# Optimization experiments

Hardware: AMD Instinct MI355X
Metric: run time of the kernel (lower is better)

## Reference

```python
import jax, jax.numpy as jnp
import numpy as np
from jax import lax

DN = ('NCHW', 'OIHW', 'NCHW')
BN_EPS = 1e-5


def _conv(x, w, pad):
    # pad: list of (lo, hi) for H, W
    return lax.conv_general_dilated(x, w, (1, 1), pad, dimension_numbers=DN)


def _grid_sample_bilinear(img, grid):
    """F.grid_sample(img, grid, align_corners=True, padding_mode='zeros').
    img: [N,C,H,W], grid: [N,Ho,Wo,2] with (x,y) in [-1,1]."""
    N, C, H, W = img.shape
    gx, gy = grid[..., 0], grid[..., 1]
    # align_corners=True mapping to pixel coords
    ix = (gx + 1.0) * 0.5 * (W - 1)
    iy = (gy + 1.0) * 0.5 * (H - 1)
    x0 = jnp.floor(ix)
    y0 = jnp.floor(iy)
    x1 = x0 + 1.0
    y1 = y0 + 1.0
    # bilinear weights
    wa = (x1 - ix) * (y1 - iy)  # top-left (x0,y0)
    wb = (ix - x0) * (y1 - iy)  # top-right (x1,y0)
    wc = (x1 - ix) * (iy - y0)  # bottom-left (x0,y1)
    wd = (ix - x0) * (iy - y0)  # bottom-right (x1,y1)

    imgc = jnp.transpose(img, (0, 2, 3, 1))  # [N,H,W,C]
    b = jnp.arange(N)[:, None, None]

    def gather(xi, yi):
        valid = (xi >= 0) & (xi <= W - 1) & (yi >= 0) & (yi <= H - 1)
        xc = jnp.clip(xi, 0, W - 1).astype(jnp.int32)
        yc = jnp.clip(yi, 0, H - 1).astype(jnp.int32)
        v = imgc[b, yc, xc]  # [N,Ho,Wo,C]
        return v * valid[..., None].astype(img.dtype)

    out = (gather(x0, y0) * wa[..., None] + gather(x1, y0) * wb[..., None]
           + gather(x0, y1) * wc[..., None] + gather(x1, y1) * wd[..., None])
    return jnp.transpose(out, (0, 3, 1, 2))  # [N,C,Ho,Wo]


def setup_inputs() -> dict:
    key = jax.random.key(0)
    ks = jax.random.split(key, 12)
    N, C1, C2 = 8, 512, 256
    H, W = 64, 64
    x1 = jax.random.normal(ks[0], (N, C1, 2 * H, 2 * W), dtype=jnp.float32)
    x2 = jax.random.normal(ks[1], (N, C2, H, W), dtype=jnp.float32)
    w_change = jax.random.normal(ks[2], (C2, C1, 1, 1), dtype=jnp.float32) * 0.02
    b_change = jax.random.normal(ks[3], (C2,), dtype=jnp.float32) * 0.02
    w_cc1 = jax.random.normal(ks[4], (C2, 2 * C2, 1, 1), dtype=jnp.float32) * 0.02
    bn_gamma = 1.0 + 0.1 * jax.random.normal(ks[5], (C2,), dtype=jnp.float32)
    bn_beta = 0.1 * jax.random.normal(ks[6], (C2,), dtype=jnp.float32)
    bn_mean = 0.1 * jax.random.normal(ks[7], (C2,), dtype=jnp.float32)
    bn_var = jax.random.uniform(ks[8], (C2,), dtype=jnp.float32, minval=0.5, maxval=1.5)
    w_cc2 = jax.random.normal(ks[9], (4, C2, 3, 3), dtype=jnp.float32) * 0.02
    return {"x1": x1, "x2": x2, "w_change": w_change, "b_change": b_change,
            "w_cc1": w_cc1, "bn_gamma": bn_gamma, "bn_beta": bn_beta,
            "bn_mean": bn_mean, "bn_var": bn_var, "w_cc2": w_cc2}


def reference(x1, x2, w_change, b_change, w_cc1, bn_gamma, bn_beta, bn_mean, bn_var, w_cc2):
    # MaxPool2d(2,2)
    x1p = lax.reduce_window(x1, -jnp.inf, lax.max, (1, 1, 2, 2), (1, 1, 2, 2), 'VALID')
    # change: 1x1 conv with bias
    x1c = _conv(x1p, w_change, [(0, 0), (0, 0)]) + b_change[None, :, None, None]
    # concat + concat_conv (1x1 conv -> BN(eval) -> ReLU -> 3x3 conv)
    x = jnp.concatenate([x1c, x2], axis=1)
    x = _conv(x, w_cc1, [(0, 0), (0, 0)])
    inv = lax.rsqrt(bn_var + BN_EPS)
    x = (x - bn_mean[None, :, None, None]) * (inv * bn_gamma)[None, :, None, None] + bn_beta[None, :, None, None]
    x = jax.nn.relu(x)
    flow = _conv(x, w_cc2, [(1, 1), (1, 1)])  # [N,4,H,W]
    flow1 = flow[:, :2]
    flow2 = flow[:, 2:]

    N, _, H, W = x1c.shape
    # base grid: [...,0]=x over width, [...,1]=y over height
    xs = jnp.linspace(-1.0, 1.0, W, dtype=x1c.dtype)
    ys = jnp.linspace(-1.0, 1.0, H, dtype=x1c.dtype)
    base = jnp.stack(jnp.meshgrid(xs, ys, indexing='xy'), axis=-1)  # [H,W,2]
    norm = jnp.array([(W - 1) / 2.0, (H - 1) / 2.0], dtype=x1c.dtype)

    grid1 = base[None] + jnp.transpose(flow1, (0, 2, 3, 1)) / norm
    grid2 = base[None] + jnp.transpose(flow2, (0, 2, 3, 1)) / norm

    u1 = _grid_sample_bilinear(x1c, grid1)
    u2 = _grid_sample_bilinear(x2, grid2)
    return u1 + u2
```

## Files before the change

kernel.cpp:

```cpp
#include <hip/hip_runtime.h>
#include <hip/hip_bf16.h>

#define NB 8
#define C1 512
#define C2 256
#define HWSZ 4096
#define BN_EPS 1e-5f
#define P2 264

typedef __hip_bfloat16 bf16;
typedef __hip_bfloat162 bf162;
typedef __attribute__((ext_vector_type(8))) short short8v;
typedef __attribute__((ext_vector_type(4))) float f32x4;

static __device__ inline float b2f(bf16 h) { return __bfloat162float(h); }

static __device__ inline unsigned short f2bf(float f) {
  union { bf16 h; unsigned short u; } c;
  c.h = __float2bfloat16(f);
  return c.u;
}

static __device__ inline unsigned pack2(float a, float b) {
  union { unsigned u; bf162 h; } pk;
  pk.h = __float22bfloat162_rn(make_float2(a, b));
  return pk.u;
}

static __device__ inline uint2 pack4(float a, float b, float c, float d) {
  union { uint2 u; bf162 h[2]; } pk;
  pk.h[0] = __float22bfloat162_rn(make_float2(a, b));
  pk.h[1] = __float22bfloat162_rn(make_float2(c, d));
  return pk.u;
}

#define SBARQ() asm volatile("s_waitcnt lgkmcnt(0)\n\ts_barrier" ::: "memory")
#define SBAR()  asm volatile("s_barrier" ::: "memory")
#define LGKM0() asm volatile("s_waitcnt lgkmcnt(0)" ::: "memory")

__global__ __launch_bounds__(256) void k0_swizzle(
    const float* __restrict__ wch, const float* __restrict__ wcc1,
    unsigned short* __restrict__ wchB, unsigned short* __restrict__ wcc1B) {
  const int t = blockIdx.x * 256 + threadIdx.x;
  const int which = t >> 17;
  const int r = t & 131071;
  const int i = r & 7;
  const int lane = (r >> 3) & 63;
  const int ntile = (r >> 9) & 15;
  const int kstep = r >> 13;
  const int ci = kstep * 32 + (lane >> 4) * 8 + i;
  const int co = ntile * 16 + (lane & 15);
  const float* s = which ? wcc1 : wch;
  unsigned short* d = which ? wcc1B : wchB;
  d[r] = f2bf(s[co * 512 + ci]);
}

__global__ __launch_bounds__(256) void k12_fused(
    const float* __restrict__ x1, const float* __restrict__ x2,
    const unsigned short* __restrict__ wchB, const unsigned short* __restrict__ wcc1B,
    const float* __restrict__ bch,
    const float* __restrict__ gamma, const float* __restrict__ beta,
    const float* __restrict__ mean, const float* __restrict__ var,
    bf16* __restrict__ x1c, bf16* __restrict__ xbn) {
  __shared__ unsigned short As[32 * 40];
  __shared__ unsigned short As2[32 * P2];
  const int tid = threadIdx.x;
  const int lane = tid & 63;
  const int wv = tid >> 6;
  const int lrow = lane & 15;
  const int lgrp = lane >> 4;

  const int m0g = blockIdx.x * 32;
  const int n = m0g >> 12;
  const int hw0 = m0g & 4095;
  const int h = hw0 >> 6;
  const int w0 = hw0 & 63;

  f32x4 acc[2][4];
#pragma unroll
  for (int mt = 0; mt < 2; ++mt)
#pragma unroll
    for (int nt = 0; nt < 4; ++nt) acc[mt][nt] = (f32x4){0.f, 0.f, 0.f, 0.f};

  const int pmi = tid & 15;
  const int ms = pmi * 2;
  const int ch0 = (tid >> 4) * 2;

  const float* x1p = x1 + (size_t)n * C1 * 16384 + (size_t)(2 * h) * 128 + 2 * (w0 + ms);

  float4 t0, b0, t1, b1;
#define LOADA(K0_) do { \
    const float* p_ = x1p + (size_t)((K0_) + ch0) * 16384; \
    t0 = *(const float4*)p_;            b0 = *(const float4*)(p_ + 128); \
    t1 = *(const float4*)(p_ + 16384);  b1 = *(const float4*)(p_ + 16384 + 128); \
  } while (0)
#define POOLA(U0_, U1_) do { \
    U0_ = pack2(fmaxf(fmaxf(t0.x, t0.y), fmaxf(b0.x, b0.y)), \
                fmaxf(fmaxf(t1.x, t1.y), fmaxf(b1.x, b1.y))); \
    U1_ = pack2(fmaxf(fmaxf(t0.z, t0.w), fmaxf(b0.z, b0.w)), \
                fmaxf(fmaxf(t1.z, t1.w), fmaxf(b1.z, b1.w))); \
  } while (0)

  unsigned uA0, uA1;
  LOADA(0);
  POOLA(uA0, uA1);
  LOADA(32);

  for (int ks = 0; ks < 16; ++ks) {
    SBARQ();
    *(unsigned*)&As[ms * 40 + ch0] = uA0;
    *(unsigned*)&As[(ms + 1) * 40 + ch0] = uA1;
    LGKM0();
    SBAR();

    unsigned uN0, uN1;
    if (ks < 15) {
      POOLA(uN0, uN1);
      if (ks < 14) LOADA((ks + 2) * 32);
    }

    const short8v a0 = *(const short8v*)&As[lrow * 40 + lgrp * 8];
    const short8v a1 = *(const short8v*)&As[(16 + lrow) * 40 + lgrp * 8];
#pragma unroll
    for (int nt = 0; nt < 4; ++nt) {
      const int ntile = wv * 4 + nt;
      const short8v b = *(const short8v*)&wchB[(size_t)((ks * 16 + ntile) * 64 + lane) * 8];
      acc[0][nt] = __builtin_amdgcn_mfma_f32_16x16x32_bf16(a0, b, acc[0][nt], 0, 0, 0);
      acc[1][nt] = __builtin_amdgcn_mfma_f32_16x16x32_bf16(a1, b, acc[1][nt], 0, 0, 0);
    }
    if (ks < 15) { uA0 = uN0; uA1 = uN1; }
  }

  const int chB = tid >> 3;
  const int mqB = (tid & 7) * 4;
  float4 cf0 = *(const float4*)&x2[((size_t)(n * C2 + chB)) * HWSZ + hw0 + mqB];
  float4 cf1 = *(const float4*)&x2[((size_t)(n * C2 + 32 + chB)) * HWSZ + hw0 + mqB];

#pragma unroll
  for (int nt = 0; nt < 4; ++nt) {
    const int co = wv * 64 + nt * 16 + lrow;
    const float bias = bch[co];
#pragma unroll
    for (int mt = 0; mt < 2; ++mt) {
      const f32x4 v = acc[mt][nt];
      const uint2 pk = pack4(v.x + bias, v.y + bias, v.z + bias, v.w + bias);
      *(uint2*)&x1c[((size_t)(n * C2 + co)) * HWSZ + hw0 + mt * 16 + lgrp * 4] = pk;
      const int mb = mt * 16 + lgrp * 4;
      As2[(mb + 0) * P2 + co] = (unsigned short)(pk.x & 0xffffu);
      As2[(mb + 1) * P2 + co] = (unsigned short)(pk.x >> 16);
      As2[(mb + 2) * P2 + co] = (unsigned short)(pk.y & 0xffffu);
      As2[(mb + 3) * P2 + co] = (unsigned short)(pk.y >> 16);
      acc[mt][nt] = (f32x4){0.f, 0.f, 0.f, 0.f};
    }
  }
  LGKM0();
  SBAR();

#pragma unroll
  for (int ks = 0; ks < 8; ++ks) {
    const short8v a0 = *(const short8v*)&As2[lrow * P2 + ks * 32 + lgrp * 8];
    const short8v a1 = *(const short8v*)&As2[(16 + lrow) * P2 + ks * 32 + lgrp * 8];
#pragma unroll
    for (int nt = 0; nt < 4; ++nt) {
      const int ntile = wv * 4 + nt;
      const short8v b = *(const short8v*)&wcc1B[(size_t)((ks * 16 + ntile) * 64 + lane) * 8];
      acc[0][nt] = __builtin_amdgcn_mfma_f32_16x16x32_bf16(a0, b, acc[0][nt], 0, 0, 0);
      acc[1][nt] = __builtin_amdgcn_mfma_f32_16x16x32_bf16(a1, b, acc[1][nt], 0, 0, 0);
    }
  }

  for (int ks = 8; ks < 16; ++ks) {
    const unsigned p0 = pack2(cf0.x, cf0.y);
    const unsigned p1 = pack2(cf0.z, cf0.w);
    cf0 = cf1;
    if (ks < 14) {
      cf1 = *(const float4*)&x2[((size_t)(n * C2 + (ks - 6) * 32 + chB)) * HWSZ + hw0 + mqB];
    }
    SBARQ();
    As[(mqB + 0) * 40 + chB] = (unsigned short)(p0 & 0xffffu);
    As[(mqB + 1) * 40 + chB] = (unsigned short)(p0 >> 16);
    As[(mqB + 2) * 40 + chB] = (unsigned short)(p1 & 0xffffu);
    As[(mqB + 3) * 40 + chB] = (unsigned short)(p1 >> 16);
    LGKM0();
    SBAR();

    const short8v a0 = *(const short8v*)&As[lrow * 40 + lgrp * 8];
    const short8v a1 = *(const short8v*)&As[(16 + lrow) * 40 + lgrp * 8];
#pragma unroll
    for (int nt = 0; nt < 4; ++nt) {
      const int ntile = wv * 4 + nt;
      const short8v b = *(const short8v*)&wcc1B[(size_t)((ks * 16 + ntile) * 64 + lane) * 8];
      acc[0][nt] = __builtin_amdgcn_mfma_f32_16x16x32_bf16(a0, b, acc[0][nt], 0, 0, 0);
      acc[1][nt] = __builtin_amdgcn_mfma_f32_16x16x32_bf16(a1, b, acc[1][nt], 0, 0, 0);
    }
  }

#pragma unroll
  for (int nt = 0; nt < 4; ++nt) {
    const int co = wv * 64 + nt * 16 + lrow;
    const float sc = gamma[co] * rsqrtf(var[co] + BN_EPS);
    const float sh = beta[co] - mean[co] * sc;
#pragma unroll
    for (int mt = 0; mt < 2; ++mt) {
      const f32x4 vv = acc[mt][nt];
      *(uint2*)&xbn[((size_t)(n * C2 + co)) * HWSZ + hw0 + mt * 16 + lgrp * 4] =
          pack4(fmaxf(vv.x * sc + sh, 0.f), fmaxf(vv.y * sc + sh, 0.f),
                fmaxf(vv.z * sc + sh, 0.f), fmaxf(vv.w * sc + sh, 0.f));
    }
  }
#undef LOADA
#undef POOLA
}

__global__ __launch_bounds__(1024) void k34_conv_sample(
    const bf16* __restrict__ xbn, const float* __restrict__ wcc2,
    const bf16* __restrict__ x1c, const float* __restrict__ x2,
    float* __restrict__ out) {
  __shared__ float wsm[9216];
  __shared__ float part[16][4][64];
  __shared__ float flr[4][64];
  const int tid = threadIdx.x;
  const int n = blockIdx.x >> 6;
  const int h = blockIdx.x & 63;
  const int wl = tid & 63;
  const int q = tid >> 6;

  for (int idx = tid; idx < 9216; idx += 1024) {
    const int f = idx / 2304;
    const int r = idx % 2304;
    const int ci = r / 9;
    const int t = r % 9;
    wsm[ci * 36 + (t / 3) * 12 + (t % 3) * 4 + f] = wcc2[idx];
  }
  __syncthreads();

  float acc[4] = {0.f, 0.f, 0.f, 0.f};
  {
    const bf16* base = xbn + ((size_t)(n * C2 + q * 16)) * HWSZ;
    const float* wq = wsm + (q * 16) * 36;
    for (int cc = 0; cc < 16; ++cc) {
      const bf16* src = base + (size_t)cc * HWSZ;
      const float* wc = wq + cc * 36;
#pragma unroll
      for (int dy = 0; dy < 3; ++dy) {
        const int y = h + dy - 1;
        if ((unsigned)y >= 64u) continue;
        const float v = b2f(src[y * 64 + wl]);
        float vm = __shfl_up(v, 1);
        float vp = __shfl_down(v, 1);
        if (wl == 0) vm = 0.f;
        if (wl == 63) vp = 0.f;
        const float4 wa = *(const float4*)&wc[dy * 12 + 0];
        const float4 wb = *(const float4*)&wc[dy * 12 + 4];
        const float4 wd = *(const float4*)&wc[dy * 12 + 8];
        acc[0] = fmaf(vm, wa.x, fmaf(v, wb.x, fmaf(vp, wd.x, acc[0])));
        acc[1] = fmaf(vm, wa.y, fmaf(v, wb.y, fmaf(vp, wd.y, acc[1])));
        acc[2] = fmaf(vm, wa.z, fmaf(v, wb.z, fmaf(vp, wd.z, acc[2])));
        acc[3] = fmaf(vm, wa.w, fmaf(v, wb.w, fmaf(vp, wd.w, acc[3])));
      }
    }
  }
  part[q][0][wl] = acc[0];
  part[q][1][wl] = acc[1];
  part[q][2][wl] = acc[2];
  part[q][3][wl] = acc[3];
  __syncthreads();
  if (tid < 256) {
    const int f = tid >> 6;
    const int ww = tid & 63;
    float s = 0.f;
#pragma unroll
    for (int qq = 0; qq < 16; ++qq) s += part[qq][f][ww];
    flr[f][ww] = s;
  }
  __syncthreads();

  const float fx1 = flr[0][wl];
  const float fy1 = flr[1][wl];
  const float fx2 = flr[2][wl];
  const float fy2 = flr[3][wl];

  int oA1, oB1, oC1, oD1; float wa1, wb1, wc1, wd1;
  {
    const float ix = (float)wl + fx1, iy = (float)h + fy1;
    const float x0f = floorf(ix), y0f = floorf(iy);
    const float fx = ix - x0f, fy = iy - y0f;
    const int x0 = (int)x0f, y0 = (int)y0f, x1i = x0 + 1, y1i = y0 + 1;
    const float vx0 = (x0 >= 0 && x0 < 64) ? 1.f : 0.f;
    const float vx1 = (x1i >= 0 && x1i < 64) ? 1.f : 0.f;
    const float vy0 = (y0 >= 0 && y0 < 64) ? 1.f : 0.f;
    const float vy1 = (y1i >= 0 && y1i < 64) ? 1.f : 0.f;
    const int cx0 = min(max(x0, 0), 63), cx1 = min(max(x1i, 0), 63);
    const int cy0 = min(max(y0, 0), 63), cy1 = min(max(y1i, 0), 63);
    oA1 = cy0 * 64 + cx0; oB1 = cy0 * 64 + cx1;
    oC1 = cy1 * 64 + cx0; oD1 = cy1 * 64 + cx1;
    wa1 = (1.f - fx) * (1.f - fy) * vx0 * vy0;
    wb1 = fx * (1.f - fy) * vx1 * vy0;
    wc1 = (1.f - fx) * fy * vx0 * vy1;
    wd1 = fx * fy * vx1 * vy1;
  }
  int oA2, oB2, oC2, oD2; float wa2, wb2, wc2, wd2;
  {
    const float ix = (float)wl + fx2, iy = (float)h + fy2;
    const float x0f = floorf(ix), y0f = floorf(iy);
    const float fx = ix - x0f, fy = iy - y0f;
    const int x0 = (int)x0f, y0 = (int)y0f, x1i = x0 + 1, y1i = y0 + 1;
    const float vx0 = (x0 >= 0 && x0 < 64) ? 1.f : 0.f;
    const float vx1 = (x1i >= 0 && x1i < 64) ? 1.f : 0.f;
    const float vy0 = (y0 >= 0 && y0 < 64) ? 1.f : 0.f;
    const float vy1 = (y1i >= 0 && y1i < 64) ? 1.f : 0.f;
    const int cx0 = min(max(x0, 0), 63), cx1 = min(max(x1i, 0), 63);
    const int cy0 = min(max(y0, 0), 63), cy1 = min(max(y1i, 0), 63);
    oA2 = cy0 * 64 + cx0; oB2 = cy0 * 64 + cx1;
    oC2 = cy1 * 64 + cx0; oD2 = cy1 * 64 + cx1;
    wa2 = (1.f - fx) * (1.f - fy) * vx0 * vy0;
    wb2 = fx * (1.f - fy) * vx1 * vy0;
    wc2 = (1.f - fx) * fy * vx0 * vy1;
    wd2 = fx * fy * vx1 * vy1;
  }

  const bf16*  p1 = x1c + ((size_t)n * C2) * HWSZ;
  const float* p2 = x2 + ((size_t)n * C2) * HWSZ;
  const size_t obase = ((size_t)n * C2) * HWSZ + h * 64 + wl;
#pragma unroll 4
  for (int i = 0; i < 16; ++i) {
    const int co = q * 16 + i;
    const bf16*  q1 = p1 + (size_t)co * HWSZ;
    const float* q2 = p2 + (size_t)co * HWSZ;
    const float u = b2f(q1[oA1]) * wa1 + b2f(q1[oB1]) * wb1 + b2f(q1[oC1]) * wc1 + b2f(q1[oD1]) * wd1
                  + q2[oA2] * wa2 + q2[oB2] * wb2 + q2[oC2] * wc2 + q2[oD2] * wd2;
    out[obase + (size_t)co * HWSZ] = u;
  }
}

extern "C" void kernel_launch(void* const* d_in, const int* in_sizes, int n_in,
                              void* d_out, int out_size, void* d_ws, size_t ws_size,
                              hipStream_t stream) {
  const float* x1      = (const float*)d_in[0];
  const float* x2      = (const float*)d_in[1];
  const float* w_change= (const float*)d_in[2];
  const float* b_change= (const float*)d_in[3];
  const float* w_cc1   = (const float*)d_in[4];
  const float* bn_gamma= (const float*)d_in[5];
  const float* bn_beta = (const float*)d_in[6];
  const float* bn_mean = (const float*)d_in[7];
  const float* bn_var  = (const float*)d_in[8];
  const float* w_cc2   = (const float*)d_in[9];
  float* out = (float*)d_out;

  bf16*           x1c   = (bf16*)d_ws;
  bf16*           xbn   = (bf16*)((char*)d_ws + (16u << 20));
  unsigned short* wchB  = (unsigned short*)((char*)d_ws + (32u << 20));
  unsigned short* wcc1B = (unsigned short*)((char*)d_ws + (32u << 20) + (256u << 10));

  k0_swizzle<<<1024, 256, 0, stream>>>(w_change, w_cc1, wchB, wcc1B);
  k12_fused<<<1024, 256, 0, stream>>>(x1, x2, wchB, wcc1B, b_change,
                                      bn_gamma, bn_beta, bn_mean, bn_var,
                                      x1c, xbn);
  k34_conv_sample<<<512, 1024, 0, stream>>>(xbn, w_cc2, x1c, x2, out);
}
```

Baseline: 146.2 us.

## Double-buffer LDS A tile and deepen x1 prefetch to remove a barrier

Splits the shared A staging tile into two buffers alternated by iteration parity, so each k-step needs one barrier instead of two. The x1 global loads move from a two-stage to a three-stage prefetch using two register sets, hiding more memory latency behind the MFMA work. In exchange it uses more registers and LDS. Correctness relies on the single barrier per step stopping a buffer from being overwritten while another wave still reads it.

Result: slower. 154.2 us (+5.5%).

```diff
diff --git a/kernel.cpp b/kernel.cpp
--- a/kernel.cpp
+++ b/kernel.cpp
@@ -34,7 +34,7 @@
   return pk.u;
 }
 
-#define SBARQ() asm volatile("s_waitcnt lgkmcnt(0)\n\ts_barrier" ::: "memory")
+#define LBAR()  asm volatile("s_waitcnt lgkmcnt(0)\n\ts_barrier" ::: "memory")
 #define SBAR()  asm volatile("s_barrier" ::: "memory")
 #define LGKM0() asm volatile("s_waitcnt lgkmcnt(0)" ::: "memory")
 
@@ -62,7 +62,7 @@
     const float* __restrict__ gamma, const float* __restrict__ beta,
     const float* __restrict__ mean, const float* __restrict__ var,
     bf16* __restrict__ x1c, bf16* __restrict__ xbn) {
-  __shared__ unsigned short As[32 * 40];
+  __shared__ unsigned short As[2][32 * 40];
   __shared__ unsigned short As2[32 * P2];
   const int tid = threadIdx.x;
   const int lane = tid & 63;
@@ -88,39 +88,45 @@
 
   const float* x1p = x1 + (size_t)n * C1 * 16384 + (size_t)(2 * h) * 128 + 2 * (w0 + ms);
 
-  float4 t0, b0, t1, b1;
-#define LOADA(K0_) do { \
+  float4 t0a, b0a, t1a, b1a, t0b, b0b, t1b, b1b;
+#define LOADA(K0_, S_) do { \
     const float* p_ = x1p + (size_t)((K0_) + ch0) * 16384; \
-    t0 = *(const float4*)p_;            b0 = *(const float4*)(p_ + 128); \
-    t1 = *(const float4*)(p_ + 16384);  b1 = *(const float4*)(p_ + 16384 + 128); \
+    t0##S_ = *(const float4*)p_;            b0##S_ = *(const float4*)(p_ + 128); \
+    t1##S_ = *(const float4*)(p_ + 16384);  b1##S_ = *(const float4*)(p_ + 16384 + 128); \
   } while (0)
-#define POOLA(U0_, U1_) do { \
-    U0_ = pack2(fmaxf(fmaxf(t0.x, t0.y), fmaxf(b0.x, b0.y)), \
-                fmaxf(fmaxf(t1.x, t1.y), fmaxf(b1.x, b1.y))); \
-    U1_ = pack2(fmaxf(fmaxf(t0.z, t0.w), fmaxf(b0.z, b0.w)), \
-                fmaxf(fmaxf(t1.z, t1.w), fmaxf(b1.z, b1.w))); \
+#define POOLA(S_, U0_, U1_) do { \
+    U0_ = pack2(fmaxf(fmaxf(t0##S_.x, t0##S_.y), fmaxf(b0##S_.x, b0##S_.y)), \
+                fmaxf(fmaxf(t1##S_.x, t1##S_.y), fmaxf(b1##S_.x, b1##S_.y))); \
+    U1_ = pack2(fmaxf(fmaxf(t0##S_.z, t0##S_.w), fmaxf(b0##S_.z, b0##S_.w)), \
+                fmaxf(fmaxf(t1##S_.z, t1##S_.w), fmaxf(b1##S_.z, b1##S_.w))); \
   } while (0)
 
-  unsigned uA0, uA1;
-  LOADA(0);
-  POOLA(uA0, uA1);
-  LOADA(32);
-
+  unsigned uC0, uC1;
+  LOADA(0, a);
+  LOADA(32, b);
+  POOLA(a, uC0, uC1);
+  LOADA(64, a);
+
+#pragma unroll 2
   for (int ks = 0; ks < 16; ++ks) {
-    SBARQ();
-    *(unsigned*)&As[ms * 40 + ch0] = uA0;
-    *(unsigned*)&As[(ms + 1) * 40 + ch0] = uA1;
-    LGKM0();
-    SBAR();
-
-    unsigned uN0, uN1;
+    unsigned short* Ab = As[ks & 1];
+    *(unsigned*)&Ab[ms * 40 + ch0] = uC0;
+    *(unsigned*)&Ab[(ms + 1) * 40 + ch0] = uC1;
+    LBAR();
+
+    unsigned uN0 = 0, uN1 = 0;
     if (ks < 15) {
-      POOLA(uN0, uN1);
-      if (ks < 14) LOADA((ks + 2) * 32);
-    }
-
-    const short8v a0 = *(const short8v*)&As[lrow * 40 + lgrp * 8];
-    const short8v a1 = *(const short8v*)&As[(16 + lrow) * 40 + lgrp * 8];
+      if ((ks & 1) == 0) {
+        POOLA(b, uN0, uN1);
+        if (ks <= 12) LOADA((ks + 3) * 32, b);
+      } else {
+        POOLA(a, uN0, uN1);
+        if (ks <= 12) LOADA((ks + 3) * 32, a);
+      }
+    }
+
+    const short8v a0 = *(const short8v*)&Ab[lrow * 40 + lgrp * 8];
+    const short8v a1 = *(const short8v*)&Ab[(16 + lrow) * 40 + lgrp * 8];
 #pragma unroll
     for (int nt = 0; nt < 4; ++nt) {
       const int ntile = wv * 4 + nt;
@@ -128,7 +134,7 @@
       acc[0][nt] = __builtin_amdgcn_mfma_f32_16x16x32_bf16(a0, b, acc[0][nt], 0, 0, 0);
       acc[1][nt] = __builtin_amdgcn_mfma_f32_16x16x32_bf16(a1, b, acc[1][nt], 0, 0, 0);
     }
-    if (ks < 15) { uA0 = uN0; uA1 = uN1; }
+    uC0 = uN0; uC1 = uN1;
   }
 
   const int chB = tid >> 3;
@@ -153,8 +159,7 @@
       acc[mt][nt] = (f32x4){0.f, 0.f, 0.f, 0.f};
     }
   }
-  LGKM0();
-  SBAR();
+  LBAR();
 
 #pragma unroll
   for (int ks = 0; ks < 8; ++ks) {
@@ -176,16 +181,15 @@
     if (ks < 14) {
       cf1 = *(const float4*)&x2[((size_t)(n * C2 + (ks - 6) * 32 + chB)) * HWSZ + hw0 + mqB];
     }
-    SBARQ();
-    As[(mqB + 0) * 40 + chB] = (unsigned short)(p0 & 0xffffu);
-    As[(mqB + 1) * 40 + chB] = (unsigned short)(p0 >> 16);
-    As[(mqB + 2) * 40 + chB] = (unsigned short)(p1 & 0xffffu);
-    As[(mqB + 3) * 40 + chB] = (unsigned short)(p1 >> 16);
-    LGKM0();
-    SBAR();
-
-    const short8v a0 = *(const short8v*)&As[lrow * 40 + lgrp * 8];
-    const short8v a1 = *(const short8v*)&As[(16 + lrow) * 40 + lgrp * 8];
+    unsigned short* Ab = As[ks & 1];
+    Ab[(mqB + 0) * 40 + chB] = (unsigned short)(p0 & 0xffffu);
+    Ab[(mqB + 1) * 40 + chB] = (unsigned short)(p0 >> 16);
+    Ab[(mqB + 2) * 40 + chB] = (unsigned short)(p1 & 0xffffu);
+    Ab[(mqB + 3) * 40 + chB] = (unsigned short)(p1 >> 16);
+    LBAR();
+
+    const short8v a0 = *(const short8v*)&Ab[lrow * 40 + lgrp * 8];
+    const short8v a1 = *(const short8v*)&Ab[(16 + lrow) * 40 + lgrp * 8];
 #pragma unroll
     for (int nt = 0; nt < 4; ++nt) {
       const int ntile = wv * 4 + nt;
```

## Double the fused GEMM block tile to 64 pixels with 8 waves

Applied to the files above, without the earlier changes.

The fused pool+1x1-conv+concat-conv kernel now processes 64 spatial positions per block (a full image row) with 512 threads. Each wave covers 4 M-tiles by 2 N-tiles instead of 2 by 4, so each weight fragment loaded from global memory feeds twice as many MFMAs. The intent is to halve redundant weight traffic and reduce the block count. The cost is more LDS per block (roughly doubled As2), more accumulator registers per wave, and half as many blocks for occupancy.

Measured after the change: 141.5 us. 1.03x faster.

```diff
diff --git a/kernel.cpp b/kernel.cpp
--- a/kernel.cpp
+++ b/kernel.cpp
@@ -55,38 +55,37 @@
   d[r] = f2bf(s[co * 512 + ci]);
 }
 
-__global__ __launch_bounds__(256) void k12_fused(
+__global__ __launch_bounds__(512) void k12_fused(
     const float* __restrict__ x1, const float* __restrict__ x2,
     const unsigned short* __restrict__ wchB, const unsigned short* __restrict__ wcc1B,
     const float* __restrict__ bch,
     const float* __restrict__ gamma, const float* __restrict__ beta,
     const float* __restrict__ mean, const float* __restrict__ var,
     bf16* __restrict__ x1c, bf16* __restrict__ xbn) {
-  __shared__ unsigned short As[32 * 40];
-  __shared__ unsigned short As2[32 * P2];
+  __shared__ unsigned short As[64 * 40];
+  __shared__ unsigned short As2[64 * P2];
   const int tid = threadIdx.x;
   const int lane = tid & 63;
   const int wv = tid >> 6;
   const int lrow = lane & 15;
   const int lgrp = lane >> 4;
 
-  const int m0g = blockIdx.x * 32;
+  const int m0g = blockIdx.x * 64;
   const int n = m0g >> 12;
   const int hw0 = m0g & 4095;
   const int h = hw0 >> 6;
-  const int w0 = hw0 & 63;
-
-  f32x4 acc[2][4];
-#pragma unroll
-  for (int mt = 0; mt < 2; ++mt)
-#pragma unroll
-    for (int nt = 0; nt < 4; ++nt) acc[mt][nt] = (f32x4){0.f, 0.f, 0.f, 0.f};
-
-  const int pmi = tid & 15;
+
+  f32x4 acc[4][2];
+#pragma unroll
+  for (int mt = 0; mt < 4; ++mt)
+#pragma unroll
+    for (int nt = 0; nt < 2; ++nt) acc[mt][nt] = (f32x4){0.f, 0.f, 0.f, 0.f};
+
+  const int pmi = tid & 31;
   const int ms = pmi * 2;
-  const int ch0 = (tid >> 4) * 2;
-
-  const float* x1p = x1 + (size_t)n * C1 * 16384 + (size_t)(2 * h) * 128 + 2 * (w0 + ms);
+  const int ch0 = (tid >> 5) * 2;
+
+  const float* x1p = x1 + (size_t)n * C1 * 16384 + (size_t)(2 * h) * 128 + 2 * ms;
 
   float4 t0, b0, t1, b1;
 #define LOADA(K0_) do { \
@@ -119,29 +118,32 @@
       if (ks < 14) LOADA((ks + 2) * 32);
     }
 
-    const short8v a0 = *(const short8v*)&As[lrow * 40 + lgrp * 8];
-    const short8v a1 = *(const short8v*)&As[(16 + lrow) * 40 + lgrp * 8];
-#pragma unroll
-    for (int nt = 0; nt < 4; ++nt) {
-      const int ntile = wv * 4 + nt;
+    short8v a[4];
+#pragma unroll
+    for (int mt = 0; mt < 4; ++mt)
+      a[mt] = *(const short8v*)&As[(mt * 16 + lrow) * 40 + lgrp * 8];
+#pragma unroll
+    for (int nt = 0; nt < 2; ++nt) {
+      const int ntile = wv * 2 + nt;
       const short8v b = *(const short8v*)&wchB[(size_t)((ks * 16 + ntile) * 64 + lane) * 8];
-      acc[0][nt] = __builtin_amdgcn_mfma_f32_16x16x32_bf16(a0, b, acc[0][nt], 0, 0, 0);
-      acc[1][nt] = __builtin_amdgcn_mfma_f32_16x16x32_bf16(a1, b, acc[1][nt], 0, 0, 0);
+#pragma unroll
+      for (int mt = 0; mt < 4; ++mt)
+        acc[mt][nt] = __builtin_amdgcn_mfma_f32_16x16x32_bf16(a[mt], b, acc[mt][nt], 0, 0, 0);
     }
     if (ks < 15) { uA0 = uN0; uA1 = uN1; }
   }
 
-  const int chB = tid >> 3;
-  const int mqB = (tid & 7) * 4;
+  const int chB = tid >> 4;
+  const int mqB = (tid & 15) * 4;
   float4 cf0 = *(const float4*)&x2[((size_t)(n * C2 + chB)) * HWSZ + hw0 + mqB];
   float4 cf1 = *(const float4*)&x2[((size_t)(n * C2 + 32 + chB)) * HWSZ + hw0 + mqB];
 
 #pragma unroll
-  for (int nt = 0; nt < 4; ++nt) {
-    const int co = wv * 64 + nt * 16 + lrow;
+  for (int nt = 0; nt < 2; ++nt) {
+    const int co = (wv * 2 + nt) * 16 + lrow;
     const float bias = bch[co];
 #pragma unroll
-    for (int mt = 0; mt < 2; ++mt) {
+    for (int mt = 0; mt < 4; ++mt) {
       const f32x4 v = acc[mt][nt];
       const uint2 pk = pack4(v.x + bias, v.y + bias, v.z + bias, v.w + bias);
       *(uint2*)&x1c[((size_t)(n * C2 + co)) * HWSZ + hw0 + mt * 16 + lgrp * 4] = pk;
@@ -158,14 +160,17 @@
 
 #pragma unroll
   for (int ks = 0; ks < 8; ++ks) {
-    const short8v a0 = *(const short8v*)&As2[lrow * P2 + ks * 32 + lgrp * 8];
-    const short8v a1 = *(const short8v*)&As2[(16 + lrow) * P2 + ks * 32 + lgrp * 8];
-#pragma unroll
-    for (int nt = 0; nt < 4; ++nt) {
-      const int ntile = wv * 4 + nt;
+    short8v a[4];
+#pragma unroll
+    for (int mt = 0; mt < 4; ++mt)
+      a[mt] = *(const short8v*)&As2[(mt * 16 + lrow) * P2 + ks * 32 + lgrp * 8];
+#pragma unroll
+    for (int nt = 0; nt < 2; ++nt) {
+      const int ntile = wv * 2 + nt;
       const short8v b = *(const short8v*)&wcc1B[(size_t)((ks * 16 + ntile) * 64 + lane) * 8];
-      acc[0][nt] = __builtin_amdgcn_mfma_f32_16x16x32_bf16(a0, b, acc[0][nt], 0, 0, 0);
-      acc[1][nt] = __builtin_amdgcn_mfma_f32_16x16x32_bf16(a1, b, acc[1][nt], 0, 0, 0);
+#pragma unroll
+      for (int mt = 0; mt < 4; ++mt)
+        acc[mt][nt] = __builtin_amdgcn_mfma_f32_16x16x32_bf16(a[mt], b, acc[mt][nt], 0, 0, 0);
     }
   }
 
@@ -184,24 +189,27 @@
     LGKM0();
     SBAR();
 
-    const short8v a0 = *(const short8v*)&As[lrow * 40 + lgrp * 8];
-    const short8v a1 = *(const short8v*)&As[(16 + lrow) * 40 + lgrp * 8];
-#pragma unroll
-    for (int nt = 0; nt < 4; ++nt) {
-      const int ntile = wv * 4 + nt;
+    short8v a[4];
+#pragma unroll
+    for (int mt = 0; mt < 4; ++mt)
+      a[mt] = *(const short8v*)&As[(mt * 16 + lrow) * 40 + lgrp * 8];
+#pragma unroll
+    for (int nt = 0; nt < 2; ++nt) {
+      const int ntile = wv * 2 + nt;
       const short8v b = *(const short8v*)&wcc1B[(size_t)((ks * 16 + ntile) * 64 + lane) * 8];
-      acc[0][nt] = __builtin_amdgcn_mfma_f32_16x16x32_bf16(a0, b, acc[0][nt], 0, 0, 0);
-      acc[1][nt] = __builtin_amdgcn_mfma_f32_16x16x32_bf16(a1, b, acc[1][nt], 0, 0, 0);
-    }
-  }
-
-#pragma unroll
-  for (int nt = 0; nt < 4; ++nt) {
-    const int co = wv * 64 + nt * 16 + lrow;
+#pragma unroll
+      for (int mt = 0; mt < 4; ++mt)
+        acc[mt][nt] = __builtin_amdgcn_mfma_f32_16x16x32_bf16(a[mt], b, acc[mt][nt], 0, 0, 0);
+    }
+  }
+
+#pragma unroll
+  for (int nt = 0; nt < 2; ++nt) {
+    const int co = (wv * 2 + nt) * 16 + lrow;
     const float sc = gamma[co] * rsqrtf(var[co] + BN_EPS);
     const float sh = beta[co] - mean[co] * sc;
 #pragma unroll
-    for (int mt = 0; mt < 2; ++mt) {
+    for (int mt = 0; mt < 4; ++mt) {
       const f32x4 vv = acc[mt][nt];
       *(uint2*)&xbn[((size_t)(n * C2 + co)) * HWSZ + hw0 + mt * 16 + lgrp * 4] =
           pack4(fmaxf(vv.x * sc + sh, 0.f), fmaxf(vv.y * sc + sh, 0.f),
@@ -354,8 +362,8 @@
   unsigned short* wcc1B = (unsigned short*)((char*)d_ws + (32u << 20) + (256u << 10));
 
   k0_swizzle<<<1024, 256, 0, stream>>>(w_change, w_cc1, wchB, wcc1B);
-  k12_fused<<<1024, 256, 0, stream>>>(x1, x2, wchB, wcc1B, b_change,
-                                      bn_gamma, bn_beta, bn_mean, bn_var,
-                                      x1c, xbn);
+  k12_fused<<<512, 512, 0, stream>>>(x1, x2, wchB, wcc1B, b_change,
+                                     bn_gamma, bn_beta, bn_mean, bn_var,
+                                     x1c, xbn);
   k34_conv_sample<<<512, 1024, 0, stream>>>(xbn, w_cc2, x1c, x2, out);
 }
```
